# Optimization experiments

Measured on AMD Instinct MI355X. Metric: run time of the kernel, lower is better.

## Reference

```python
import jax, jax.numpy as jnp
import numpy as np

N = 8192
IN_F = 256
HEADS = 4
HF = 64            # head_features = out_features / heads
OUT_F = HEADS * HF # concat=True
NEG_SLOPE = 0.2


def setup_inputs() -> dict:
    key = jax.random.key(0)
    ks = jax.random.split(key, 7)
    x = jax.random.normal(ks[0], (N, IN_F), dtype=jnp.float32)
    graph = jax.random.randint(ks[1], (N, N), 0, 2, dtype=jnp.int32)
    weight = jax.random.normal(ks[2], (HEADS, IN_F, HF), dtype=jnp.float32) * (1.0 / np.sqrt(IN_F))
    weight_i = jax.random.normal(ks[3], (HEADS, HF, 1), dtype=jnp.float32) * (1.0 / np.sqrt(HF))
    weight_j = jax.random.normal(ks[4], (HEADS, HF, 1), dtype=jnp.float32) * (1.0 / np.sqrt(HF))
    weight_r = jax.random.normal(ks[5], (IN_F, HF * HEADS), dtype=jnp.float32) * (1.0 / np.sqrt(IN_F))
    bias = jnp.zeros((OUT_F,), dtype=jnp.float32)
    return {"x": x, "graph": graph, "weight": weight, "weight_i": weight_i,
            "weight_j": weight_j, "weight_r": weight_r, "bias": bias}


def reference(x, graph, weight, weight_i, weight_j, weight_r, bias):
    # h: per-head projected features [heads, N, hf]
    h = jnp.einsum('nm,hmf->hnf', x, weight)
    # additive attention logits: coe_i [h,N,1] + coe_j [h,1,N]
    coe_i = jnp.einsum('hnf,hfo->hno', h, weight_i)          # [heads, N, 1]
    coe_j = jnp.einsum('hnf,hfo->hno', h, weight_j)          # [heads, N, 1]
    coe = jax.nn.leaky_relu(coe_i + jnp.swapaxes(coe_j, 1, 2), NEG_SLOPE)  # [heads, N, N]
    # adjacency mask (note transpose, matching the torch code)
    mask = jnp.where(graph > 0, 0.0, -jnp.inf).T             # [N, N]
    att = jax.nn.softmax(coe + mask[None], axis=-1)          # [heads, N, N]
    # aggregate and move heads to axis 1: [N, heads, hf]
    y = jnp.einsum('hij,hjf->ihf', att, h)
    # residual with projection (in_features != head_features)
    y = y + (x @ weight_r).reshape(N, HEADS, HF)
    # concat heads + bias
    y = y.reshape(N, OUT_F) + bias
    return y
```

## Files before the change

### kernel.cpp

```cpp
#include <hip/hip_runtime.h>
#include <hip/hip_bf16.h>

#define N 8192
#define IN_F 256
#define HEADS 4
#define HF 64
#define OUT_F 256

typedef __attribute__((ext_vector_type(8))) short short8;
typedef __attribute__((ext_vector_type(4))) float f32x4;

__device__ __forceinline__ float lrelu(float x) {
    return fmaxf(x, 0.0f) * 0.8f + x * 0.2f;
}
__device__ __forceinline__ short f2bf(float f) {
    union { __hip_bfloat16 h; short s; } u;
    u.h = __float2bfloat16(f);
    return u.s;
}
__device__ __forceinline__ float bf2f(unsigned short b) {
    union { unsigned u; float f; } v; v.u = ((unsigned)b) << 16;
    return v.f;
}
__device__ __forceinline__ unsigned pack_bf16(float p0, float p1) {
    union { __hip_bfloat162 b; unsigned u; } cv;
    cv.b = __float22bfloat162_rn(make_float2(p0, p1));
    return cv.u;
}

#define GLOAD_LDS(gsrc, ldst) \
    __builtin_amdgcn_global_load_lds( \
        (const __attribute__((address_space(1))) void*)(gsrc), \
        (__attribute__((address_space(3))) void*)(ldst), 16, 0, 0)

__global__ __launch_bounds__(256) void k_wcvt(
    const float* __restrict__ w, const float* __restrict__ wr,
    unsigned short* __restrict__ BbT)
{
    int c = blockIdx.x;
    int k = threadIdx.x;
    float v;
    if (c < 256) {
        int head = c >> 6, f = c & 63;
        v = w[((size_t)head * IN_F + k) * HF + f];
    } else {
        v = wr[(size_t)k * OUT_F + (c - 256)];
    }
    BbT[(size_t)c * IN_F + k] = (unsigned short)f2bf(v);
}

__global__ __launch_bounds__(256) void k_gemm_pack(
    const float* __restrict__ x, const unsigned short* __restrict__ BbT,
    const float* __restrict__ bias, const float* __restrict__ wi,
    const float* __restrict__ wj,
    unsigned short* __restrict__ hT, float* __restrict__ out,
    float* __restrict__ coe_i, float* __restrict__ coe_j,
    const int* __restrict__ graph, unsigned int* __restrict__ bits)
{
    __shared__ unsigned short Asw[64 * 64];
    __shared__ unsigned short Bsw[128 * 64];
    int b = blockIdx.x;
    int t = threadIdx.x;

    if (b >= 512) {
        int p = b - 512;
        int jw = p & 255;
        int i = (p >> 8) * 256 + t;
        const int* gp = graph + (size_t)(jw * 32) * N + i;
        unsigned int word = 0;
        #pragma unroll
        for (int k = 0; k < 32; ++k)
            word |= (gp[(size_t)k * N] > 0 ? 1u : 0u) << k;
        bits[(size_t)jw * N + i] = word;
        return;
    }

    int m0 = (b & 127) * 64;
    int bn = b >> 7;
    int w_ = t >> 6, l = t & 63;
    int wr_ = w_ >> 1, wc_ = w_ & 1;
    int ar = l & 15, g = l >> 4;

    f32x4 acc[2][4];
    #pragma unroll
    for (int m = 0; m < 2; ++m)
        #pragma unroll
        for (int n = 0; n < 4; ++n) acc[m][n] = (f32x4){0.f, 0.f, 0.f, 0.f};

    int srow = t >> 2, skq = (t & 3) * 16;
    int sc = t >> 1, sh = (t & 1) * 32;

    for (int kt = 0; kt < 4; ++kt) {
        const float* xs = x + (size_t)(m0 + srow) * IN_F + kt * 64 + skq;
        float4 xa = ((const float4*)xs)[0];
        float4 xb = ((const float4*)xs)[1];
        float4 xc = ((const float4*)xs)[2];
        float4 xd = ((const float4*)xs)[3];
        unsigned ae[8];
        ae[0] = pack_bf16(xa.x, xa.y); ae[1] = pack_bf16(xa.z, xa.w);
        ae[2] = pack_bf16(xb.x, xb.y); ae[3] = pack_bf16(xb.z, xb.w);
        ae[4] = pack_bf16(xc.x, xc.y); ae[5] = pack_bf16(xc.z, xc.w);
        ae[6] = pack_bf16(xd.x, xd.y); ae[7] = pack_bf16(xd.z, xd.w);
        int kb0 = (skq >> 3) ^ (srow & 7);
        int kb1 = ((skq >> 3) + 1) ^ (srow & 7);
        *(uint4*)&Asw[srow * 64 + kb0 * 8] = *(uint4*)&ae[0];
        *(uint4*)&Asw[srow * 64 + kb1 * 8] = *(uint4*)&ae[4];
        const unsigned short* bs = BbT + (size_t)(bn * 128 + sc) * IN_F + kt * 64 + sh;
        uint4 b0 = ((const uint4*)bs)[0];
        uint4 b1 = ((const uint4*)bs)[1];
        uint4 b2 = ((const uint4*)bs)[2];
        uint4 b3 = ((const uint4*)bs)[3];
        int hb = sh >> 3;
        *(uint4*)&Bsw[sc * 64 + ((hb + 0) ^ (sc & 7)) * 8] = b0;
        *(uint4*)&Bsw[sc * 64 + ((hb + 1) ^ (sc & 7)) * 8] = b1;
        *(uint4*)&Bsw[sc * 64 + ((hb + 2) ^ (sc & 7)) * 8] = b2;
        *(uint4*)&Bsw[sc * 64 + ((hb + 3) ^ (sc & 7)) * 8] = b3;
        __syncthreads();
        #pragma unroll
        for (int ks = 0; ks < 2; ++ks) {
            short8 af[2], bf[4];
            #pragma unroll
            for (int m = 0; m < 2; ++m) {
                int row = wr_ * 32 + m * 16 + ar;
                int kb = (ks * 4 + g) ^ (row & 7);
                af[m] = *(const short8*)&Asw[row * 64 + kb * 8];
            }
            #pragma unroll
            for (int n = 0; n < 4; ++n) {
                int c = wc_ * 64 + n * 16 + ar;
                int kb = (ks * 4 + g) ^ (c & 7);
                bf[n] = *(const short8*)&Bsw[c * 64 + kb * 8];
            }
            #pragma unroll
            for (int m = 0; m < 2; ++m)
                #pragma unroll
                for (int n = 0; n < 4; ++n)
                    acc[m][n] = __builtin_amdgcn_mfma_f32_16x16x32_bf16(af[m], bf[n], acc[m][n], 0, 0, 0);
        }
        __syncthreads();
    }
    #pragma unroll
    for (int m = 0; m < 2; ++m) {
        #pragma unroll
        for (int n = 0; n < 4; ++n) {
            int cg = bn * 128 + wc_ * 64 + n * 16 + ar;
            int mg0 = m0 + wr_ * 32 + m * 16 + g * 4;
            if (cg < 256) {
                int head = cg >> 6, f = cg & 63;
                unsigned pk[2];
                pk[0] = pack_bf16(acc[m][n][0], acc[m][n][1]);
                pk[1] = pack_bf16(acc[m][n][2], acc[m][n][3]);
                *(uint2*)(hT + (size_t)(head * HF + f) * N + mg0) = *(uint2*)pk;
            } else {
                float bb = bias[cg - 256];
                #pragma unroll
                for (int r = 0; r < 4; ++r)
                    out[(size_t)(mg0 + r) * OUT_F + (cg - 256)] = acc[m][n][r] + bb;
            }
        }
    }
    if (bn < 2) {
        int head = bn * 2 + wc_;
        float pi[2][4], pj[2][4];
        #pragma unroll
        for (int m = 0; m < 2; ++m)
            #pragma unroll
            for (int r = 0; r < 4; ++r) { pi[m][r] = 0.f; pj[m][r] = 0.f; }
        #pragma unroll
        for (int n = 0; n < 4; ++n) {
            float wiv = wi[head * HF + n * 16 + ar];
            float wjv = wj[head * HF + n * 16 + ar];
            #pragma unroll
            for (int m = 0; m < 2; ++m)
                #pragma unroll
                for (int r = 0; r < 4; ++r) {
                    pi[m][r] = fmaf(acc[m][n][r], wiv, pi[m][r]);
                    pj[m][r] = fmaf(acc[m][n][r], wjv, pj[m][r]);
                }
        }
        #pragma unroll
        for (int o = 1; o <= 8; o <<= 1)
            #pragma unroll
            for (int m = 0; m < 2; ++m)
                #pragma unroll
                for (int r = 0; r < 4; ++r) {
                    pi[m][r] += __shfl_xor(pi[m][r], o, 64);
                    pj[m][r] += __shfl_xor(pj[m][r], o, 64);
                }
        if (ar == 0) {
            #pragma unroll
            for (int m = 0; m < 2; ++m)
                #pragma unroll
                for (int r = 0; r < 4; ++r) {
                    int row = m0 + wr_ * 32 + m * 16 + g * 4 + r;
                    coe_i[head * N + row] = pi[m][r];
                    coe_j[head * N + row] = pj[m][r];
                }
        }
    }
}

__global__ __launch_bounds__(256) void k_cols(
    const float* __restrict__ coe_j, float* __restrict__ maxB,
    float* __restrict__ F, float* __restrict__ H)
{
    __shared__ float red[256];
    int head = blockIdx.x;
    int t = threadIdx.x;
    float m = -1e30f;
    for (int n = t; n < N; n += 256) {
        float b = coe_j[head * N + n];
        F[head * N + n] = __expf(b);
        H[head * N + n] = __expf(0.2f * b);
        m = fmaxf(m, b);
    }
    red[t] = m;
    __syncthreads();
    for (int s = 128; s > 0; s >>= 1) {
        if (t < s) red[t] = fmaxf(red[t], red[t + s]);
        __syncthreads();
    }
    if (t == 0) maxB[head] = red[0];
}

__device__ __forceinline__ short8 makeP(
    const float4& fa, const float4& fb4, const float4& ha, const float4& hb4,
    unsigned int mk, float Ei, float Gi)
{
    float fv[8] = {fa.x, fa.y, fa.z, fa.w, fb4.x, fb4.y, fb4.z, fb4.w};
    float hv[8] = {ha.x, ha.y, ha.z, ha.w, hb4.x, hb4.y, hb4.z, hb4.w};
    union { short8 s8; unsigned u[4]; } A;
    #pragma unroll
    for (int jp = 0; jp < 4; ++jp) {
        float p0 = fmaxf(Ei * fv[2 * jp],     Gi * hv[2 * jp]);
        float p1 = fmaxf(Ei * fv[2 * jp + 1], Gi * hv[2 * jp + 1]);
        int s0 = __builtin_amdgcn_sbfe((int)mk, 2 * jp, 1);
        int s1 = __builtin_amdgcn_sbfe((int)mk, 2 * jp + 1, 1);
        p0 = __int_as_float(__float_as_int(p0) & s0);
        p1 = __int_as_float(__float_as_int(p1) & s1);
        A.u[jp] = pack_bf16(p0, p1);
    }
    return A.s8;
}

__global__ __launch_bounds__(512) void k_att(
    const unsigned short* __restrict__ hT, const float* __restrict__ coe_i,
    const float* __restrict__ maxB, const float* __restrict__ F,
    const float* __restrict__ H, const unsigned int* __restrict__ bits,
    float* __restrict__ out)
{
    __shared__ char smem[65536];
    unsigned short* hb = (unsigned short*)smem;
    float* mbuf = (float*)smem;

    int t = threadIdx.x;
    int head = blockIdx.y;
    int i0 = blockIdx.x * 64;
    int w = t >> 6, l = t & 63;
    int rg = w >> 2, grp = w & 3;
    int ar = l & 15, g = l >> 4, g8 = g * 8;

    int irow0 = i0 + rg * 32 + ar;
    int irow1 = irow0 + 16;
    float mB = maxB[head];
    float a0 = coe_i[head * N + irow0];
    float a1 = coe_i[head * N + irow1];
    float M0 = lrelu(a0 + mB);
    float M1 = lrelu(a1 + mB);
    float Ei0 = __expf(a0 - M0), Gi0 = __expf(0.2f * a0 - M0);
    float Ei1 = __expf(a1 - M1), Gi1 = __expf(0.2f * a1 - M1);

    f32x4 acc0[4], acc1[4];
    #pragma unroll
    for (int fb = 0; fb < 4; ++fb) {
        acc0[fb] = (f32x4){0.f, 0.f, 0.f, 0.f};
        acc1[fb] = (f32x4){0.f, 0.f, 0.f, 0.f};
    }
    f32x4 accd0 = (f32x4){0.f, 0.f, 0.f, 0.f};
    f32x4 accd1 = (f32x4){0.f, 0.f, 0.f, 0.f};

    short8 ones;
    #pragma unroll
    for (int k = 0; k < 8; ++k) ones[k] = (short)0x3F80;

    int tg = w >> 1;
    int rb0 = (w & 1) * 32;
    int lrow = l >> 3;
    int slot = l & 7;
    int gg = slot ^ lrow;
    const unsigned short* qsrc[4];
    #pragma unroll
    for (int q = 0; q < 4; ++q) {
        int sf = rb0 + q * 8 + lrow;
        qsrc[q] = hT + (size_t)(head * HF + sf) * N + tg * 64 + gg * 8;
    }
    int ldsoff0 = tg * 4096 + rb0 * 64;

    const float* Fp = F + head * N + g8;
    const float* Hp = H + head * N + g8;
    const unsigned int* bp0 = bits + irow0;
    const unsigned int* bp1 = bits + irow1;

    #pragma unroll
    for (int q = 0; q < 4; ++q)
        GLOAD_LDS(qsrc[q], hb + ldsoff0 + q * 512);
    unsigned mk00, mk01, mk10, mk11;
    {
        int jt0 = grp * 64;
        size_t jw0 = (size_t)(jt0 >> 5);
        mk00 = bp0[jw0 * N] >> g8;
        mk01 = bp0[(jw0 + 1) * N] >> g8;
        mk10 = bp1[jw0 * N] >> g8;
        mk11 = bp1[(jw0 + 1) * N] >> g8;
    }

    for (int s = 0; s < 32; ++s) {
        int jt = s * 256 + grp * 64;
        float4 fa0 = *(const float4*)(Fp + jt);
        float4 fb0 = *(const float4*)(Fp + jt + 4);
        float4 ha0 = *(const float4*)(Hp + jt);
        float4 hb0 = *(const float4*)(Hp + jt + 4);
        float4 fa1 = *(const float4*)(Fp + jt + 32);
        float4 fb1 = *(const float4*)(Fp + jt + 36);
        float4 ha1 = *(const float4*)(Hp + jt + 32);
        float4 hb1 = *(const float4*)(Hp + jt + 36);
        short8 af00 = makeP(fa0, fb0, ha0, hb0, mk00, Ei0, Gi0);
        short8 af10 = makeP(fa0, fb0, ha0, hb0, mk10, Ei1, Gi1);
        short8 af01 = makeP(fa1, fb1, ha1, hb1, mk01, Ei0, Gi0);
        short8 af11 = makeP(fa1, fb1, ha1, hb1, mk11, Ei1, Gi1);

        __syncthreads();

        if (s < 31) {
            int bon = ((s + 1) & 1) * 16384;
            int jn = (s + 1) * 256;
            #pragma unroll
            for (int q = 0; q < 4; ++q)
                GLOAD_LDS(qsrc[q] + jn, hb + bon + ldsoff0 + q * 512);
        }
        int sn = (s + 1 < 32) ? s + 1 : s;
        size_t jwn = (size_t)(((size_t)sn * 256 + grp * 64) >> 5);
        unsigned nk00 = bp0[jwn * N] >> g8;
        unsigned nk01 = bp0[(jwn + 1) * N] >> g8;
        unsigned nk10 = bp1[jwn * N] >> g8;
        unsigned nk11 = bp1[(jwn + 1) * N] >> g8;

        int bo = (s & 1) * 16384;
        const unsigned short* rbuf = &hb[bo + grp * 4096];
        #pragma unroll
        for (int ss = 0; ss < 2; ++ss) {
            short8 a0f = ss ? af01 : af00;
            short8 a1f = ss ? af11 : af10;
            #pragma unroll
            for (int fb = 0; fb < 4; ++fb) {
                int row = fb * 16 + ar;
                int pg = (ss * 4 + g) ^ (ar & 7);
                short8 bfr = *(const short8*)&rbuf[row * 64 + pg * 8];
                acc0[fb] = __builtin_amdgcn_mfma_f32_16x16x32_bf16(a0f, bfr, acc0[fb], 0, 0, 0);
                acc1[fb] = __builtin_amdgcn_mfma_f32_16x16x32_bf16(a1f, bfr, acc1[fb], 0, 0, 0);
            }
            accd0 = __builtin_amdgcn_mfma_f32_16x16x32_bf16(a0f, ones, accd0, 0, 0, 0);
            accd1 = __builtin_amdgcn_mfma_f32_16x16x32_bf16(a1f, ones, accd1, 0, 0, 0);
        }
        mk00 = nk00; mk01 = nk01; mk10 = nk10; mk11 = nk11;
    }

    __syncthreads();
    int slot_m = rg * 64 + l;
    if (grp > 0) {
        float* dst = mbuf + (size_t)(grp - 1) * 5248 + slot_m * 41;
        #pragma unroll
        for (int fb = 0; fb < 4; ++fb)
            #pragma unroll
            for (int r = 0; r < 4; ++r) {
                dst[fb * 4 + r] = acc0[fb][r];
                dst[16 + fb * 4 + r] = acc1[fb][r];
            }
        #pragma unroll
        for (int r = 0; r < 4; ++r) {
            dst[32 + r] = accd0[r];
            dst[36 + r] = accd1[r];
        }
    }
    __syncthreads();
    if (grp == 0) {
        #pragma unroll
        for (int q = 0; q < 3; ++q) {
            const float* src = mbuf + (size_t)q * 5248 + slot_m * 41;
            #pragma unroll
            for (int fb = 0; fb < 4; ++fb)
                #pragma unroll
                for (int r = 0; r < 4; ++r) {
                    acc0[fb][r] += src[fb * 4 + r];
                    acc1[fb][r] += src[16 + fb * 4 + r];
                }
            #pragma unroll
            for (int r = 0; r < 4; ++r) {
                accd0[r] += src[32 + r];
                accd1[r] += src[36 + r];
            }
        }
        #pragma unroll
        for (int r = 0; r < 4; ++r) {
            float inv0 = 1.0f / accd0[r];
            float inv1 = 1.0f / accd1[r];
            int orow0 = i0 + rg * 32 + g * 4 + r;
            float* op0 = out + (size_t)orow0 * OUT_F + head * HF + ar;
            float* op1 = op0 + 16 * OUT_F;
            #pragma unroll
            for (int fb = 0; fb < 4; ++fb) {
                op0[fb * 16] += acc0[fb][r] * inv0;
                op1[fb * 16] += acc1[fb][r] * inv1;
            }
        }
    }
}

extern "C" void kernel_launch(void* const* d_in, const int* in_sizes, int n_in,
                              void* d_out, int out_size, void* d_ws, size_t ws_size,
                              hipStream_t stream) {
    const float* x     = (const float*)d_in[0];
    const int*   graph = (const int*)d_in[1];
    const float* w     = (const float*)d_in[2];
    const float* wi    = (const float*)d_in[3];
    const float* wj    = (const float*)d_in[4];
    const float* wr    = (const float*)d_in[5];
    const float* bias  = (const float*)d_in[6];
    float* out = (float*)d_out;

    char* ws = (char*)d_ws;
    unsigned short* hT  = (unsigned short*)(ws);
    float* coe_i = (float*)(ws + 4194304);
    float* coe_j = (float*)(ws + 4325376);
    float* maxB  = (float*)(ws + 4456448);
    float* F     = (float*)(ws + 4457472);
    float* H     = (float*)(ws + 4588544);
    unsigned short* BbT = (unsigned short*)(ws + 4719616);
    unsigned int* bits  = (unsigned int*)(ws + 4981760);

    k_wcvt<<<dim3(512), 256, 0, stream>>>(w, wr, BbT);
    k_gemm_pack<<<dim3(512 + 8192), 256, 0, stream>>>(x, BbT, bias, wi, wj, hT, out, coe_i, coe_j, graph, bits);
    k_cols<<<dim3(4), 256, 0, stream>>>(coe_j, maxB, F, H);
    k_att<<<dim3(N / 64, HEADS), 512, 0, stream>>>(hT, coe_i, maxB, F, H, bits, out);
}
```

Baseline: 157.9 us.

## Split attention j-range across waves with private LDS buffers and tree merge

```diff
diff --git a/kernel.cpp b/kernel.cpp
--- a/kernel.cpp
+++ b/kernel.cpp
@@ -32,6 +32,8 @@
     __builtin_amdgcn_global_load_lds( \
         (const __attribute__((address_space(1))) void*)(gsrc), \
         (__attribute__((address_space(3))) void*)(ldst), 16, 0, 0)
+
+#define MFMA16 __builtin_amdgcn_mfma_f32_16x16x32_bf16
 
 __global__ __launch_bounds__(256) void k_wcvt(
     const float* __restrict__ w, const float* __restrict__ wr,
@@ -135,7 +137,7 @@
             for (int m = 0; m < 2; ++m)
                 #pragma unroll
                 for (int n = 0; n < 4; ++n)
-                    acc[m][n] = __builtin_amdgcn_mfma_f32_16x16x32_bf16(af[m], bf[n], acc[m][n], 0, 0, 0);
+                    acc[m][n] = MFMA16(af[m], bf[n], acc[m][n], 0, 0, 0);
         }
         __syncthreads();
     }
@@ -243,6 +245,33 @@
     return A.s8;
 }
 
+__device__ __forceinline__ void merge_write(float* dst, f32x4 (&acc)[4][4], f32x4 (&accd)[4]) {
+    #pragma unroll
+    for (int rg = 0; rg < 4; ++rg) {
+        #pragma unroll
+        for (int fb = 0; fb < 4; ++fb)
+            #pragma unroll
+            for (int r = 0; r < 4; ++r)
+                dst[rg * 16 + fb * 4 + r] = acc[rg][fb][r];
+        #pragma unroll
+        for (int r = 0; r < 4; ++r)
+            dst[64 + rg * 4 + r] = accd[rg][r];
+    }
+}
+__device__ __forceinline__ void merge_add(const float* src, f32x4 (&acc)[4][4], f32x4 (&accd)[4]) {
+    #pragma unroll
+    for (int rg = 0; rg < 4; ++rg) {
+        #pragma unroll
+        for (int fb = 0; fb < 4; ++fb)
+            #pragma unroll
+            for (int r = 0; r < 4; ++r)
+                acc[rg][fb][r] += src[rg * 16 + fb * 4 + r];
+        #pragma unroll
+        for (int r = 0; r < 4; ++r)
+            accd[rg][r] += src[64 + rg * 4 + r];
+    }
+}
+
 __global__ __launch_bounds__(512) void k_att(
     const unsigned short* __restrict__ hT, const float* __restrict__ coe_i,
     const float* __restrict__ maxB, const float* __restrict__ F,
@@ -250,167 +279,145 @@
     float* __restrict__ out)
 {
     __shared__ char smem[65536];
-    unsigned short* hb = (unsigned short*)smem;
-    float* mbuf = (float*)smem;
 
     int t = threadIdx.x;
     int head = blockIdx.y;
     int i0 = blockIdx.x * 64;
     int w = t >> 6, l = t & 63;
-    int rg = w >> 2, grp = w & 3;
     int ar = l & 15, g = l >> 4, g8 = g * 8;
 
-    int irow0 = i0 + rg * 32 + ar;
-    int irow1 = irow0 + 16;
     float mB = maxB[head];
-    float a0 = coe_i[head * N + irow0];
-    float a1 = coe_i[head * N + irow1];
-    float M0 = lrelu(a0 + mB);
-    float M1 = lrelu(a1 + mB);
-    float Ei0 = __expf(a0 - M0), Gi0 = __expf(0.2f * a0 - M0);
-    float Ei1 = __expf(a1 - M1), Gi1 = __expf(0.2f * a1 - M1);
-
-    f32x4 acc0[4], acc1[4];
-    #pragma unroll
-    for (int fb = 0; fb < 4; ++fb) {
-        acc0[fb] = (f32x4){0.f, 0.f, 0.f, 0.f};
-        acc1[fb] = (f32x4){0.f, 0.f, 0.f, 0.f};
-    }
-    f32x4 accd0 = (f32x4){0.f, 0.f, 0.f, 0.f};
-    f32x4 accd1 = (f32x4){0.f, 0.f, 0.f, 0.f};
+    float Eiv[4], Giv[4];
+    #pragma unroll
+    for (int rg = 0; rg < 4; ++rg) {
+        float a = coe_i[head * N + i0 + rg * 16 + ar];
+        float M = lrelu(a + mB);
+        Eiv[rg] = __expf(a - M);
+        Giv[rg] = __expf(0.2f * a - M);
+    }
+
+    f32x4 acc[4][4];
+    f32x4 accd[4];
+    #pragma unroll
+    for (int rg = 0; rg < 4; ++rg) {
+        #pragma unroll
+        for (int fb = 0; fb < 4; ++fb) acc[rg][fb] = (f32x4){0.f, 0.f, 0.f, 0.f};
+        accd[rg] = (f32x4){0.f, 0.f, 0.f, 0.f};
+    }
 
     short8 ones;
     #pragma unroll
     for (int k = 0; k < 8; ++k) ones[k] = (short)0x3F80;
 
-    int tg = w >> 1;
-    int rb0 = (w & 1) * 32;
-    int lrow = l >> 3;
-    int slot = l & 7;
-    int gg = slot ^ lrow;
+    unsigned short* lbase = (unsigned short*)(smem + w * 8192);
+    int srq = l >> 2;
+    int sslot = l & 3;
     const unsigned short* qsrc[4];
     #pragma unroll
     for (int q = 0; q < 4; ++q) {
-        int sf = rb0 + q * 8 + lrow;
-        qsrc[q] = hT + (size_t)(head * HF + sf) * N + tg * 64 + gg * 8;
-    }
-    int ldsoff0 = tg * 4096 + rb0 * 64;
+        int row = q * 16 + srq;
+        int gg = sslot ^ (row & 3);
+        qsrc[q] = hT + (size_t)(head * HF + row) * N + gg * 8;
+    }
 
     const float* Fp = F + head * N + g8;
     const float* Hp = H + head * N + g8;
-    const unsigned int* bp0 = bits + irow0;
-    const unsigned int* bp1 = bits + irow1;
+    const unsigned int* bbase = bits + i0 + ar;
+
+    int j0 = w * 1024;
 
     #pragma unroll
     for (int q = 0; q < 4; ++q)
-        GLOAD_LDS(qsrc[q], hb + ldsoff0 + q * 512);
-    unsigned mk00, mk01, mk10, mk11;
+        GLOAD_LDS(qsrc[q] + j0, lbase + q * 512);
+    unsigned mk0, mk1, mk2, mk3;
+    float4 cfa, cfb, cha, chb;
     {
-        int jt0 = grp * 64;
-        size_t jw0 = (size_t)(jt0 >> 5);
-        mk00 = bp0[jw0 * N] >> g8;
-        mk01 = bp0[(jw0 + 1) * N] >> g8;
-        mk10 = bp1[jw0 * N] >> g8;
-        mk11 = bp1[(jw0 + 1) * N] >> g8;
-    }
-
+        size_t jw0 = (size_t)(j0 >> 5);
+        mk0 = bbase[jw0 * N +  0] >> g8;
+        mk1 = bbase[jw0 * N + 16] >> g8;
+        mk2 = bbase[jw0 * N + 32] >> g8;
+        mk3 = bbase[jw0 * N + 48] >> g8;
+        cfa = *(const float4*)(Fp + j0);
+        cfb = *(const float4*)(Fp + j0 + 4);
+        cha = *(const float4*)(Hp + j0);
+        chb = *(const float4*)(Hp + j0 + 4);
+    }
+
+    #pragma unroll 1
     for (int s = 0; s < 32; ++s) {
-        int jt = s * 256 + grp * 64;
-        float4 fa0 = *(const float4*)(Fp + jt);
-        float4 fb0 = *(const float4*)(Fp + jt + 4);
-        float4 ha0 = *(const float4*)(Hp + jt);
-        float4 hb0 = *(const float4*)(Hp + jt + 4);
-        float4 fa1 = *(const float4*)(Fp + jt + 32);
-        float4 fb1 = *(const float4*)(Fp + jt + 36);
-        float4 ha1 = *(const float4*)(Hp + jt + 32);
-        float4 hb1 = *(const float4*)(Hp + jt + 36);
-        short8 af00 = makeP(fa0, fb0, ha0, hb0, mk00, Ei0, Gi0);
-        short8 af10 = makeP(fa0, fb0, ha0, hb0, mk10, Ei1, Gi1);
-        short8 af01 = makeP(fa1, fb1, ha1, hb1, mk01, Ei0, Gi0);
-        short8 af11 = makeP(fa1, fb1, ha1, hb1, mk11, Ei1, Gi1);
-
-        __syncthreads();
-
-        if (s < 31) {
-            int bon = ((s + 1) & 1) * 16384;
-            int jn = (s + 1) * 256;
-            #pragma unroll
-            for (int q = 0; q < 4; ++q)
-                GLOAD_LDS(qsrc[q] + jn, hb + bon + ldsoff0 + q * 512);
-        }
-        int sn = (s + 1 < 32) ? s + 1 : s;
-        size_t jwn = (size_t)(((size_t)sn * 256 + grp * 64) >> 5);
-        unsigned nk00 = bp0[jwn * N] >> g8;
-        unsigned nk01 = bp0[(jwn + 1) * N] >> g8;
-        unsigned nk10 = bp1[jwn * N] >> g8;
-        unsigned nk11 = bp1[(jwn + 1) * N] >> g8;
-
-        int bo = (s & 1) * 16384;
-        const unsigned short* rbuf = &hb[bo + grp * 4096];
-        #pragma unroll
-        for (int ss = 0; ss < 2; ++ss) {
-            short8 a0f = ss ? af01 : af00;
-            short8 a1f = ss ? af11 : af10;
-            #pragma unroll
-            for (int fb = 0; fb < 4; ++fb) {
-                int row = fb * 16 + ar;
-                int pg = (ss * 4 + g) ^ (ar & 7);
-                short8 bfr = *(const short8*)&rbuf[row * 64 + pg * 8];
-                acc0[fb] = __builtin_amdgcn_mfma_f32_16x16x32_bf16(a0f, bfr, acc0[fb], 0, 0, 0);
-                acc1[fb] = __builtin_amdgcn_mfma_f32_16x16x32_bf16(a1f, bfr, acc1[fb], 0, 0, 0);
-            }
-            accd0 = __builtin_amdgcn_mfma_f32_16x16x32_bf16(a0f, ones, accd0, 0, 0, 0);
-            accd1 = __builtin_amdgcn_mfma_f32_16x16x32_bf16(a1f, ones, accd1, 0, 0, 0);
-        }
-        mk00 = nk00; mk01 = nk01; mk10 = nk10; mk11 = nk11;
-    }
-
-    __syncthreads();
-    int slot_m = rg * 64 + l;
-    if (grp > 0) {
-        float* dst = mbuf + (size_t)(grp - 1) * 5248 + slot_m * 41;
-        #pragma unroll
-        for (int fb = 0; fb < 4; ++fb)
+        int jt = j0 + s * 32;
+        int sn = (s + 1 < 32) ? s + 1 : 0;
+        int jtn = j0 + sn * 32;
+        #pragma unroll
+        for (int q = 0; q < 4; ++q)
+            GLOAD_LDS(qsrc[q] + jtn, lbase + ((s + 1) & 1) * 2048 + q * 512);
+        size_t jwn = (size_t)(jtn >> 5);
+        unsigned nk0 = bbase[jwn * N +  0] >> g8;
+        unsigned nk1 = bbase[jwn * N + 16] >> g8;
+        unsigned nk2 = bbase[jwn * N + 32] >> g8;
+        unsigned nk3 = bbase[jwn * N + 48] >> g8;
+        float4 nfa = *(const float4*)(Fp + jtn);
+        float4 nfb = *(const float4*)(Fp + jtn + 4);
+        float4 nha = *(const float4*)(Hp + jtn);
+        float4 nhb = *(const float4*)(Hp + jtn + 4);
+
+        asm volatile("s_waitcnt vmcnt(12)" ::: "memory");
+        __builtin_amdgcn_sched_barrier(0);
+
+        short8 af0 = makeP(cfa, cfb, cha, chb, mk0, Eiv[0], Giv[0]);
+        short8 af1 = makeP(cfa, cfb, cha, chb, mk1, Eiv[1], Giv[1]);
+        short8 af2 = makeP(cfa, cfb, cha, chb, mk2, Eiv[2], Giv[2]);
+        short8 af3 = makeP(cfa, cfb, cha, chb, mk3, Eiv[3], Giv[3]);
+
+        const unsigned short* rbuf = lbase + (s & 1) * 2048;
+        #pragma unroll
+        for (int fb = 0; fb < 4; ++fb) {
+            int row = fb * 16 + ar;
+            int pg = g ^ (ar & 3);
+            short8 bfr = *(const short8*)&rbuf[row * 32 + pg * 8];
+            acc[0][fb] = MFMA16(af0, bfr, acc[0][fb], 0, 0, 0);
+            acc[1][fb] = MFMA16(af1, bfr, acc[1][fb], 0, 0, 0);
+            acc[2][fb] = MFMA16(af2, bfr, acc[2][fb], 0, 0, 0);
+            acc[3][fb] = MFMA16(af3, bfr, acc[3][fb], 0, 0, 0);
+        }
+        accd[0] = MFMA16(af0, ones, accd[0], 0, 0, 0);
+        accd[1] = MFMA16(af1, ones, accd[1], 0, 0, 0);
+        accd[2] = MFMA16(af2, ones, accd[2], 0, 0, 0);
+        accd[3] = MFMA16(af3, ones, accd[3], 0, 0, 0);
+
+        mk0 = nk0; mk1 = nk1; mk2 = nk2; mk3 = nk3;
+        cfa = nfa; cfb = nfb; cha = nha; chb = nhb;
+    }
+
+    __syncthreads();
+    float* fm = (float*)smem;
+    int ls = l * 81;
+    if (w == 4 || w == 5) merge_write(fm + ((w - 4) * 64 * 81) + ls, acc, accd);
+    __syncthreads();
+    if (w < 2) merge_add(fm + (w * 64 * 81) + ls, acc, accd);
+    __syncthreads();
+    if (w == 6 || w == 7) merge_write(fm + ((w - 6) * 64 * 81) + ls, acc, accd);
+    __syncthreads();
+    if (w == 2 || w == 3) merge_add(fm + ((w - 2) * 64 * 81) + ls, acc, accd);
+    __syncthreads();
+    if (w == 2 || w == 3) merge_write(fm + ((w - 2) * 64 * 81) + ls, acc, accd);
+    __syncthreads();
+    if (w < 2) merge_add(fm + (w * 64 * 81) + ls, acc, accd);
+    __syncthreads();
+    if (w == 1) merge_write(fm + ls, acc, accd);
+    __syncthreads();
+    if (w == 0) {
+        merge_add(fm + ls, acc, accd);
+        #pragma unroll
+        for (int rg = 0; rg < 4; ++rg) {
             #pragma unroll
             for (int r = 0; r < 4; ++r) {
-                dst[fb * 4 + r] = acc0[fb][r];
-                dst[16 + fb * 4 + r] = acc1[fb][r];
-            }
-        #pragma unroll
-        for (int r = 0; r < 4; ++r) {
-            dst[32 + r] = accd0[r];
-            dst[36 + r] = accd1[r];
-        }
-    }
-    __syncthreads();
-    if (grp == 0) {
-        #pragma unroll
-        for (int q = 0; q < 3; ++q) {
-            const float* src = mbuf + (size_t)q * 5248 + slot_m * 41;
-            #pragma unroll
-            for (int fb = 0; fb < 4; ++fb)
-                #pragma unroll
-                for (int r = 0; r < 4; ++r) {
-                    acc0[fb][r] += src[fb * 4 + r];
-                    acc1[fb][r] += src[16 + fb * 4 + r];
-                }
-            #pragma unroll
-            for (int r = 0; r < 4; ++r) {
-                accd0[r] += src[32 + r];
-                accd1[r] += src[36 + r];
-            }
-        }
-        #pragma unroll
-        for (int r = 0; r < 4; ++r) {
-            float inv0 = 1.0f / accd0[r];
-            float inv1 = 1.0f / accd1[r];
-            int orow0 = i0 + rg * 32 + g * 4 + r;
-            float* op0 = out + (size_t)orow0 * OUT_F + head * HF + ar;
-            float* op1 = op0 + 16 * OUT_F;
-            #pragma unroll
-            for (int fb = 0; fb < 4; ++fb) {
-                op0[fb * 16] += acc0[fb][r] * inv0;
-                op1[fb * 16] += acc1[fb][r] * inv1;
+                float inv = 1.0f / accd[rg][r];
+                int orow = i0 + rg * 16 + g * 4 + r;
+                float* op = out + (size_t)orow * OUT_F + head * HF + ar;
+                #pragma unroll
+                for (int fb = 0; fb < 4; ++fb)
+                    op[fb * 16] += acc[rg][fb][r] * inv;
             }
         }
     }
```

Result: no change. 156.4 us (-0.9%).
